# Optimization experiments

Measured on AMD Instinct MI355X. Metric: run time of the kernel, lower is better.

The kernel has to match this reference:

```python
import jax, jax.numpy as jnp
import numpy as np

N = 10000
E = 320000
D = 64


def setup_inputs() -> dict:
    key = jax.random.key(0)
    k1, k2, k3 = jax.random.split(key, 3)
    z = jax.random.normal(k1, (N, D), dtype=jnp.float32)
    edge_index = jax.random.randint(k2, (2, E), 0, N, dtype=jnp.int64)
    W = jax.random.normal(k3, (D, D), dtype=jnp.float32) * (1.0 / np.sqrt(D))
    b = jnp.zeros((D,), dtype=jnp.float32)
    return {"z": z, "edge_index": edge_index, "W": W, "b": b}


def reference(z, edge_index, W, b):
    n = z.shape[0]
    # GCNConv defaults: add self-loops, symmetric normalization D^-1/2 A D^-1/2
    self_loop = jnp.arange(n, dtype=edge_index.dtype)
    row = jnp.concatenate([edge_index[0], self_loop])  # source nodes
    col = jnp.concatenate([edge_index[1], self_loop])  # destination nodes
    deg = jax.ops.segment_sum(jnp.ones_like(col, dtype=z.dtype), col, num_segments=n)
    dinv = jnp.where(deg > 0, jax.lax.rsqrt(deg), 0.0)
    norm = dinv[row] * dinv[col]                        # [E+N]
    h = z @ W                                           # [N, D] linear transform
    msg = h[row] * norm[:, None]                        # gather + scale
    agg = jax.ops.segment_sum(msg, col, num_segments=n) + b  # scatter-add + bias
    zr = jax.nn.relu(agg)
    return zr @ zr.T                                    # [N, N] reconstructed adjacency
```

## Files before the change

### kernel.cpp

```cpp
#include <hip/hip_runtime.h>
#include <math.h>

#define NN 10000
#define NE 320000
#define DD 64
#define TILE 128
#define NTILE 79
#define NPAD (NTILE * TILE)
#define PADROWS (NPAD - NN)
#define NPAIRS (NTILE * (NTILE + 1) / 2)

typedef __bf16 bf16x8 __attribute__((ext_vector_type(8)));
typedef float f32x4 __attribute__((ext_vector_type(4)));

#define OFF_CNT    0
#define OFF_FILL   40064
#define OFF_ROWPTR 80128
#define OFF_SRC    120192
#define OFF_DINV   1400192
#define OFF_H      1440256
#define OFF_ZR1    4000256
#define OFF_ZR2    5294592

__global__ void init_kernel(int* __restrict__ cnt, int* __restrict__ fill,
                            unsigned short* __restrict__ zr1,
                            unsigned short* __restrict__ zr2) {
    int tid = blockIdx.x * 256 + threadIdx.x;
    if (tid < NN) { cnt[tid] = 0; fill[tid] = 0; }
    if (tid < PADROWS * DD) {
        zr1[NN * DD + tid] = 0;
        zr2[NN * DD + tid] = 0;
    }
}

__global__ void count_kernel(const int* __restrict__ ei, int* __restrict__ cnt) {
    int e = blockIdx.x * 256 + threadIdx.x;
    if (e < NE) atomicAdd(&cnt[ei[NE + e]], 1);
}

__global__ void dinv_kernel(const int* __restrict__ cnt, float* __restrict__ dinv) {
    int i = blockIdx.x * 256 + threadIdx.x;
    if (i < NN) dinv[i] = rsqrtf((float)cnt[i] + 1.0f);
}

__global__ __launch_bounds__(256) void scan_kernel(const int* __restrict__ cnt,
                                                   int* __restrict__ rowptr) {
    __shared__ int partial[256];
    const int t = threadIdx.x;
    const int base = t * 40;
    int s = 0;
#pragma unroll 4
    for (int i = 0; i < 40; i++) {
        int idx = base + i;
        if (idx < NN) s += cnt[idx];
    }
    partial[t] = s;
    __syncthreads();
    for (int off = 1; off < 256; off <<= 1) {
        int v = (t >= off) ? partial[t - off] : 0;
        __syncthreads();
        partial[t] += v;
        __syncthreads();
    }
    int run = (t == 0) ? 0 : partial[t - 1];
    for (int i = 0; i < 40; i++) {
        int idx = base + i;
        if (idx < NN) { rowptr[idx] = run; run += cnt[idx]; }
    }
    if (t == 255) rowptr[NN] = partial[255];
}

__global__ void fill_kernel(const int* __restrict__ ei,
                            const int* __restrict__ rowptr,
                            int* __restrict__ fill, int* __restrict__ srcrow) {
    int e = blockIdx.x * 256 + threadIdx.x;
    if (e >= NE) return;
    int c = ei[NE + e];
    int pos = rowptr[c] + atomicAdd(&fill[c], 1);
    srcrow[pos] = ei[e];
}

__global__ __launch_bounds__(256) void h_kernel(const float* __restrict__ z,
                                                const float* __restrict__ W,
                                                float* __restrict__ h) {
    __shared__ float Ws[64 * 64];
    __shared__ float zs[4 * 64];
    const int tid = threadIdx.x;
    const int rbase = blockIdx.x * 4;
#pragma unroll
    for (int i = 0; i < 16; i++) Ws[i * 256 + tid] = W[i * 256 + tid];
    zs[tid] = z[rbase * DD + tid];
    __syncthreads();
    const int r = tid >> 6, d = tid & 63;
    float acc = 0.0f;
#pragma unroll
    for (int k = 0; k < 64; k++) acc = fmaf(zs[r * 64 + k], Ws[k * 64 + d], acc);
    h[(rbase + r) * DD + d] = acc;
}

__global__ __launch_bounds__(256) void agg_kernel(const int* __restrict__ rowptr,
                                                  const int* __restrict__ srcrow,
                                                  const float* __restrict__ dinv,
                                                  const float* __restrict__ h,
                                                  const float* __restrict__ b,
                                                  __bf16* __restrict__ zr1,
                                                  __bf16* __restrict__ zr2) {
    const int lane = threadIdx.x & 63;
    const int n = blockIdx.x * 4 + (threadIdx.x >> 6);
    if (n >= NN) return;
    int s = __builtin_amdgcn_readfirstlane(rowptr[n]);
    int e = __builtin_amdgcn_readfirstlane(rowptr[n + 1]);
    const float dc = dinv[n];
    float acc = 0.0f;
    int i = s;
    for (; i + 1 < e; i += 2) {
        int r0 = __builtin_amdgcn_readfirstlane(srcrow[i]);
        int r1 = __builtin_amdgcn_readfirstlane(srcrow[i + 1]);
        float n0 = dinv[r0] * dc, n1 = dinv[r1] * dc;
        float h0 = h[r0 * DD + lane], h1 = h[r1 * DD + lane];
        acc = fmaf(h0, n0, acc);
        acc = fmaf(h1, n1, acc);
    }
    for (; i < e; i++) {
        int r = __builtin_amdgcn_readfirstlane(srcrow[i]);
        acc = fmaf(h[r * DD + lane], dinv[r] * dc, acc);
    }
    acc = fmaf(h[n * DD + lane], dc * dc, acc) + b[lane];
    acc = acc > 0.0f ? acc : 0.0f;
    __bf16 hi = (__bf16)acc;
    float rem = acc - (float)hi;
    zr1[n * DD + lane] = hi;
    zr2[n * DD + lane] = (__bf16)rem;
}

__global__ __launch_bounds__(256) void gemm_kernel(const __bf16* __restrict__ z1,
                                                   const __bf16* __restrict__ z2,
                                                   float* __restrict__ C) {
    const int t = blockIdx.x;
    const float ff = (float)(2 * NTILE + 1);
    int bi = (int)((ff - sqrtf(ff * ff - 8.0f * (float)t)) * 0.5f);
    while ((bi + 1) * NTILE - ((bi + 1) * bi) / 2 <= t) bi++;
    while (bi * NTILE - (bi * (bi - 1)) / 2 > t) bi--;
    const int bj = bi + (t - (bi * NTILE - (bi * (bi - 1)) / 2));

    const int tid = threadIdx.x;
    const int lane = tid & 63;
    const int w = tid >> 6;
    const int wr = w >> 1, wc = w & 1;
    const int m16 = lane & 15;
    const int kq = lane >> 4;
    const int rbase = bi * TILE + wr * 64;
    const int cbase = bj * TILE + wc * 64;

    f32x4 acc[4][4] = {};

    for (int kk = 0; kk < 2; kk++) {
        const int ko = kk * 32 + kq * 8;
        bf16x8 a1[4], a2[4], b1[4], b2[4];
#pragma unroll
        for (int tt = 0; tt < 4; tt++) {
            const int ar = rbase + tt * 16 + m16;
            const int br = cbase + tt * 16 + m16;
            a1[tt] = *(const bf16x8*)&z1[ar * DD + ko];
            a2[tt] = *(const bf16x8*)&z2[ar * DD + ko];
            b1[tt] = *(const bf16x8*)&z1[br * DD + ko];
            b2[tt] = *(const bf16x8*)&z2[br * DD + ko];
        }
#pragma unroll
        for (int mt = 0; mt < 4; mt++)
#pragma unroll
            for (int nt = 0; nt < 4; nt++) {
                acc[mt][nt] = __builtin_amdgcn_mfma_f32_16x16x32_bf16(a2[mt], b1[nt], acc[mt][nt], 0, 0, 0);
                acc[mt][nt] = __builtin_amdgcn_mfma_f32_16x16x32_bf16(a1[mt], b2[nt], acc[mt][nt], 0, 0, 0);
                acc[mt][nt] = __builtin_amdgcn_mfma_f32_16x16x32_bf16(a1[mt], b1[nt], acc[mt][nt], 0, 0, 0);
            }
    }

#pragma unroll
    for (int mt = 0; mt < 4; mt++) {
        const int row0 = rbase + mt * 16 + kq * 4;
#pragma unroll
        for (int nt = 0; nt < 4; nt++) {
            const int col = cbase + nt * 16 + m16;
            if (col < NN) {
#pragma unroll
                for (int r = 0; r < 4; r++) {
                    const int row = row0 + r;
                    if (row < NN) C[(size_t)row * NN + col] = acc[mt][nt][r];
                }
            }
        }
    }

    if (bi != bj) {
#pragma unroll
        for (int mt = 0; mt < 4; mt++) {
            const int tcol0 = rbase + mt * 16 + kq * 4;
            if (tcol0 < NN) {
#pragma unroll
                for (int nt = 0; nt < 4; nt++) {
                    const int trow = cbase + nt * 16 + m16;
                    if (trow < NN)
                        *(f32x4*)&C[(size_t)trow * NN + tcol0] = acc[mt][nt];
                }
            }
        }
    }
}

extern "C" void kernel_launch(void* const* d_in, const int* in_sizes, int n_in,
                              void* d_out, int out_size, void* d_ws, size_t ws_size,
                              hipStream_t stream) {
    const float* z = (const float*)d_in[0];
    const int* ei = (const int*)d_in[1];
    const float* W = (const float*)d_in[2];
    const float* b = (const float*)d_in[3];
    float* C = (float*)d_out;

    char* ws = (char*)d_ws;
    int* cnt = (int*)(ws + OFF_CNT);
    int* fill = (int*)(ws + OFF_FILL);
    int* rowptr = (int*)(ws + OFF_ROWPTR);
    int* srcrow = (int*)(ws + OFF_SRC);
    float* dinv = (float*)(ws + OFF_DINV);
    float* h = (float*)(ws + OFF_H);
    __bf16* zr1 = (__bf16*)(ws + OFF_ZR1);
    __bf16* zr2 = (__bf16*)(ws + OFF_ZR2);

    init_kernel<<<(NN + 255) / 256, 256, 0, stream>>>(cnt, fill,
                                                      (unsigned short*)zr1,
                                                      (unsigned short*)zr2);
    count_kernel<<<(NE + 255) / 256, 256, 0, stream>>>(ei, cnt);
    dinv_kernel<<<(NN + 255) / 256, 256, 0, stream>>>(cnt, dinv);
    scan_kernel<<<1, 256, 0, stream>>>(cnt, rowptr);
    fill_kernel<<<(NE + 255) / 256, 256, 0, stream>>>(ei, rowptr, fill, srcrow);
    h_kernel<<<NN / 4, 256, 0, stream>>>(z, W, h);
    agg_kernel<<<(NN + 3) / 4, 256, 0, stream>>>(rowptr, srcrow, dinv, h, b, zr1, zr2);

    gemm_kernel<<<NPAIRS, 256, 0, stream>>>(zr1, zr2, C);
}
```

Measured before the change: 544.6 us.

## Fuse preprocessing stages into one cooperative kernel with grid syncs

Replaces seven separate preprocessing launches (init, count, dinv, scan, fill, linear transform, aggregation) with a single cooperative kernel that separates the phases with grid-wide syncs. The scan becomes a two-level block scan across 40 blocks instead of one single-block scan. The aim is to remove per-launch overhead and the serial single-block scan. Grid syncs across 1024 blocks have their own cost, and the bpart scratch aliases the h buffer, which is only safe because h is written after the scan phases. The old launch sequence is kept as a fallback if the cooperative launch fails.

```diff
diff --git a/kernel.cpp b/kernel.cpp
--- a/kernel.cpp
+++ b/kernel.cpp
@@ -1,5 +1,8 @@
 #include <hip/hip_runtime.h>
+#include <hip/hip_cooperative_groups.h>
 #include <math.h>
+
+namespace cg = cooperative_groups;
 
 #define NN 10000
 #define NE 320000
@@ -9,6 +12,7 @@
 #define NPAD (NTILE * TILE)
 #define PADROWS (NPAD - NN)
 #define NPAIRS (NTILE * (NTILE + 1) / 2)
+#define NB 1024
 
 typedef __bf16 bf16x8 __attribute__((ext_vector_type(8)));
 typedef float f32x4 __attribute__((ext_vector_type(4)));
@@ -21,6 +25,125 @@
 #define OFF_H      1440256
 #define OFF_ZR1    4000256
 #define OFF_ZR2    5294592
+
+__global__ __launch_bounds__(256, 4) void preproc_kernel(
+    const float* __restrict__ z, const int* __restrict__ ei,
+    const float* __restrict__ W, const float* __restrict__ bias,
+    int* __restrict__ cnt, int* __restrict__ fill,
+    int* __restrict__ rowptr, int* __restrict__ srcrow,
+    float* __restrict__ dinv, float* __restrict__ h,
+    int* __restrict__ bpart,
+    __bf16* __restrict__ zr1, __bf16* __restrict__ zr2)
+{
+    cg::grid_group grid = cg::this_grid();
+    const int tid = threadIdx.x;
+    const int gtid = blockIdx.x * 256 + tid;
+    const int gstride = NB * 256;
+
+    __shared__ union {
+        struct { float Ws[64 * 64]; float zs[4 * 64]; } hs;
+        int partial[256];
+    } sm;
+
+    for (int i = gtid; i < NN; i += gstride) { cnt[i] = 0; fill[i] = 0; }
+    for (int i = gtid; i < PADROWS * DD; i += gstride) {
+        ((unsigned short*)zr1)[NN * DD + i] = 0;
+        ((unsigned short*)zr2)[NN * DD + i] = 0;
+    }
+    grid.sync();
+
+    for (int e = gtid; e < NE; e += gstride) atomicAdd(&cnt[ei[NE + e]], 1);
+    grid.sync();
+
+    if (blockIdx.x < 40) {
+        const int idx = blockIdx.x * 256 + tid;
+        const int myc = (idx < NN) ? cnt[idx] : 0;
+        if (idx < NN) dinv[idx] = rsqrtf((float)myc + 1.0f);
+        sm.partial[tid] = myc;
+        __syncthreads();
+        for (int off = 1; off < 256; off <<= 1) {
+            int v = (tid >= off) ? sm.partial[tid - off] : 0;
+            __syncthreads();
+            sm.partial[tid] += v;
+            __syncthreads();
+        }
+        if (idx < NN) rowptr[idx] = sm.partial[tid] - myc;
+        if (tid == 255) bpart[blockIdx.x] = sm.partial[255];
+    }
+    grid.sync();
+
+    if (blockIdx.x == 0) {
+        const int v = (tid < 40) ? bpart[tid] : 0;
+        sm.partial[tid] = v;
+        __syncthreads();
+        for (int off = 1; off < 256; off <<= 1) {
+            int vv = (tid >= off) ? sm.partial[tid - off] : 0;
+            __syncthreads();
+            sm.partial[tid] += vv;
+            __syncthreads();
+        }
+        if (tid < 40) bpart[tid] = sm.partial[tid] - v;
+        if (tid == 0) rowptr[NN] = sm.partial[255];
+    }
+    grid.sync();
+
+    if (blockIdx.x < 40) {
+        const int idx = blockIdx.x * 256 + tid;
+        if (idx < NN) rowptr[idx] += bpart[blockIdx.x];
+    }
+    grid.sync();
+
+    for (int e = gtid; e < NE; e += gstride) {
+        int c = ei[NE + e];
+        int pos = rowptr[c] + atomicAdd(&fill[c], 1);
+        srcrow[pos] = ei[e];
+    }
+    grid.sync();
+
+    for (int i = tid; i < 4096; i += 256) sm.hs.Ws[i] = W[i];
+    for (int vb = blockIdx.x; vb < NN / 4; vb += NB) {
+        __syncthreads();
+        sm.hs.zs[tid] = z[vb * 256 + tid];
+        __syncthreads();
+        const int r = tid >> 6, d = tid & 63;
+        float acc = 0.0f;
+#pragma unroll
+        for (int k = 0; k < 64; k++)
+            acc = fmaf(sm.hs.zs[r * 64 + k], sm.hs.Ws[k * 64 + d], acc);
+        h[(vb * 4 + r) * DD + d] = acc;
+    }
+    grid.sync();
+
+    const int lane = tid & 63;
+    for (int g = blockIdx.x; g < (NN + 3) / 4; g += NB) {
+        const int n = g * 4 + (tid >> 6);
+        if (n < NN) {
+            int s = __builtin_amdgcn_readfirstlane(rowptr[n]);
+            int e = __builtin_amdgcn_readfirstlane(rowptr[n + 1]);
+            const float dc = dinv[n];
+            float acc = 0.0f;
+            int i = s;
+            for (; i + 1 < e; i += 2) {
+                int r0 = __builtin_amdgcn_readfirstlane(srcrow[i]);
+                int r1 = __builtin_amdgcn_readfirstlane(srcrow[i + 1]);
+                float n0 = dinv[r0] * dc, n1 = dinv[r1] * dc;
+                float h0 = h[r0 * DD + lane], h1 = h[r1 * DD + lane];
+                acc = fmaf(h0, n0, acc);
+                acc = fmaf(h1, n1, acc);
+            }
+            for (; i < e; i++) {
+                int r = __builtin_amdgcn_readfirstlane(srcrow[i]);
+                acc = fmaf(h[r * DD + lane], dinv[r] * dc, acc);
+            }
+            acc = fmaf(h[n * DD + lane], dc * dc, acc) + bias[lane];
+            acc = acc > 0.0f ? acc : 0.0f;
+            __bf16 hi = (__bf16)acc;
+            float rem = acc - (float)hi;
+            zr1[n * DD + lane] = hi;
+            zr2[n * DD + lane] = (__bf16)rem;
+        }
+    }
+}
 
 __global__ void init_kernel(int* __restrict__ cnt, int* __restrict__ fill,
                             unsigned short* __restrict__ zr1,
@@ -224,18 +347,28 @@
     int* srcrow = (int*)(ws + OFF_SRC);
     float* dinv = (float*)(ws + OFF_DINV);
     float* h = (float*)(ws + OFF_H);
+    int* bpart = (int*)(ws + OFF_H);
     __bf16* zr1 = (__bf16*)(ws + OFF_ZR1);
     __bf16* zr2 = (__bf16*)(ws + OFF_ZR2);
 
-    init_kernel<<<(NN + 255) / 256, 256, 0, stream>>>(cnt, fill,
-                                                      (unsigned short*)zr1,
-                                                      (unsigned short*)zr2);
-    count_kernel<<<(NE + 255) / 256, 256, 0, stream>>>(ei, cnt);
-    dinv_kernel<<<(NN + 255) / 256, 256, 0, stream>>>(cnt, dinv);
-    scan_kernel<<<1, 256, 0, stream>>>(cnt, rowptr);
-    fill_kernel<<<(NE + 255) / 256, 256, 0, stream>>>(ei, rowptr, fill, srcrow);
-    h_kernel<<<NN / 4, 256, 0, stream>>>(z, W, h);
-    agg_kernel<<<(NN + 3) / 4, 256, 0, stream>>>(rowptr, srcrow, dinv, h, b, zr1, zr2);
+    void* args[] = { (void*)&z, (void*)&ei, (void*)&W, (void*)&b,
+                     (void*)&cnt, (void*)&fill, (void*)&rowptr, (void*)&srcrow,
+                     (void*)&dinv, (void*)&h, (void*)&bpart,
+                     (void*)&zr1, (void*)&zr2 };
+    hipError_t err = hipLaunchCooperativeKernel((void*)preproc_kernel,
+                                                dim3(NB), dim3(256),
+                                                args, 0, stream);
+    if (err != hipSuccess) {
+        init_kernel<<<(NN + 255) / 256, 256, 0, stream>>>(cnt, fill,
+                                                          (unsigned short*)zr1,
+                                                          (unsigned short*)zr2);
+        count_kernel<<<(NE + 255) / 256, 256, 0, stream>>>(ei, cnt);
+        dinv_kernel<<<(NN + 255) / 256, 256, 0, stream>>>(cnt, dinv);
+        scan_kernel<<<1, 256, 0, stream>>>(cnt, rowptr);
+        fill_kernel<<<(NE + 255) / 256, 256, 0, stream>>>(ei, rowptr, fill, srcrow);
+        h_kernel<<<NN / 4, 256, 0, stream>>>(z, W, h);
+        agg_kernel<<<(NN + 3) / 4, 256, 0, stream>>>(rowptr, srcrow, dinv, h, b, zr1, zr2);
+    }
 
     gemm_kernel<<<NPAIRS, 256, 0, stream>>>(zr1, zr2, C);
 }
```

After: 1.208 ms. +121.9%, slower.

## Recompute transposed tile and stage output through LDS for coalesced nontemporal stores

Applied to the files above, without the earlier changes.

For off-diagonal tile pairs, the GEMM now recomputes the mirrored tile by swapping operands rather than storing the transpose with strided writes. Each wave stages its accumulator fragments through a shared-memory buffer so that rows can be written to global memory as contiguous 16-byte vectors, using nontemporal stores. The aim is to cut scattered scalar and strided global writes on the output-bound 400 MB store. The cost is doubled MFMA work and input loads for off-diagonal tiles, plus LDS traffic and barriers.

```diff
diff --git a/kernel.cpp b/kernel.cpp
--- a/kernel.cpp
+++ b/kernel.cpp
@@ -136,6 +136,8 @@
 __global__ __launch_bounds__(256) void gemm_kernel(const __bf16* __restrict__ z1,
                                                    const __bf16* __restrict__ z2,
                                                    float* __restrict__ C) {
+    __shared__ float T[4][32][64];
+
     const int t = blockIdx.x;
     const float ff = (float)(2 * NTILE + 1);
     int bi = (int)((ff - sqrtf(ff * ff - 8.0f * (float)t)) * 0.5f);
@@ -149,59 +151,60 @@
     const int wr = w >> 1, wc = w & 1;
     const int m16 = lane & 15;
     const int kq = lane >> 4;
-    const int rbase = bi * TILE + wr * 64;
-    const int cbase = bj * TILE + wc * 64;
-
-    f32x4 acc[4][4] = {};
-
-    for (int kk = 0; kk < 2; kk++) {
-        const int ko = kk * 32 + kq * 8;
-        bf16x8 a1[4], a2[4], b1[4], b2[4];
-#pragma unroll
-        for (int tt = 0; tt < 4; tt++) {
-            const int ar = rbase + tt * 16 + m16;
-            const int br = cbase + tt * 16 + m16;
-            a1[tt] = *(const bf16x8*)&z1[ar * DD + ko];
-            a2[tt] = *(const bf16x8*)&z2[ar * DD + ko];
-            b1[tt] = *(const bf16x8*)&z1[br * DD + ko];
-            b2[tt] = *(const bf16x8*)&z2[br * DD + ko];
+
+    const int norient = (bi == bj) ? 1 : 2;
+    for (int o = 0; o < norient; o++) {
+        const int Ab = (o == 0 ? bi : bj) * TILE + (o == 0 ? wr : wc) * 64;
+        const int Bb = (o == 0 ? bj : bi) * TILE + (o == 0 ? wc : wr) * 64;
+
+        f32x4 acc[4][4] = {};
+        for (int kk = 0; kk < 2; kk++) {
+            const int ko = kk * 32 + kq * 8;
+            bf16x8 a1[4], a2[4], b1[4], b2[4];
+#pragma unroll
+            for (int tt = 0; tt < 4; tt++) {
+                const int ar = Ab + tt * 16 + m16;
+                const int br = Bb + tt * 16 + m16;
+                a1[tt] = *(const bf16x8*)&z1[ar * DD + ko];
+                a2[tt] = *(const bf16x8*)&z2[ar * DD + ko];
+                b1[tt] = *(const bf16x8*)&z1[br * DD + ko];
+                b2[tt] = *(const bf16x8*)&z2[br * DD + ko];
+            }
+#pragma unroll
+            for (int mt = 0; mt < 4; mt++)
+#pragma unroll
+                for (int nt = 0; nt < 4; nt++) {
+                    acc[mt][nt] = __builtin_amdgcn_mfma_f32_16x16x32_bf16(a2[mt], b1[nt], acc[mt][nt], 0, 0, 0);
+                    acc[mt][nt] = __builtin_amdgcn_mfma_f32_16x16x32_bf16(a1[mt], b2[nt], acc[mt][nt], 0, 0, 0);
+                    acc[mt][nt] = __builtin_amdgcn_mfma_f32_16x16x32_bf16(a1[mt], b1[nt], acc[mt][nt], 0, 0, 0);
+                }
         }
-#pragma unroll
-        for (int mt = 0; mt < 4; mt++)
-#pragma unroll
-            for (int nt = 0; nt < 4; nt++) {
-                acc[mt][nt] = __builtin_amdgcn_mfma_f32_16x16x32_bf16(a2[mt], b1[nt], acc[mt][nt], 0, 0, 0);
-                acc[mt][nt] = __builtin_amdgcn_mfma_f32_16x16x32_bf16(a1[mt], b2[nt], acc[mt][nt], 0, 0, 0);
-                acc[mt][nt] = __builtin_amdgcn_mfma_f32_16x16x32_bf16(a1[mt], b1[nt], acc[mt][nt], 0, 0, 0);
-            }
-    }
-
-#pragma unroll
-    for (int mt = 0; mt < 4; mt++) {
-        const int row0 = rbase + mt * 16 + kq * 4;
-#pragma unroll
-        for (int nt = 0; nt < 4; nt++) {
-            const int col = cbase + nt * 16 + m16;
-            if (col < NN) {
-#pragma unroll
-                for (int r = 0; r < 4; r++) {
-                    const int row = row0 + r;
-                    if (row < NN) C[(size_t)row * NN + col] = acc[mt][nt][r];
+
+        for (int hf = 0; hf < 2; hf++) {
+            __syncthreads();
+#pragma unroll
+            for (int mh = 0; mh < 2; mh++) {
+                const int mt = hf * 2 + mh;
+                const int i0 = mh * 16 + kq * 4;
+#pragma unroll
+                for (int nt = 0; nt < 4; nt++) {
+                    const int j = nt * 16 + m16;
+#pragma unroll
+                    for (int r = 0; r < 4; r++)
+                        T[w][i0 + r][j] = acc[mt][nt][r];
                 }
             }
-        }
-    }
-
-    if (bi != bj) {
-#pragma unroll
-        for (int mt = 0; mt < 4; mt++) {
-            const int tcol0 = rbase + mt * 16 + kq * 4;
-            if (tcol0 < NN) {
-#pragma unroll
-                for (int nt = 0; nt < 4; nt++) {
-                    const int trow = cbase + nt * 16 + m16;
-                    if (trow < NN)
-                        *(f32x4*)&C[(size_t)trow * NN + tcol0] = acc[mt][nt];
+            __syncthreads();
+            const int rg = lane >> 4;
+            const int c0 = (lane & 15) * 4;
+#pragma unroll
+            for (int it = 0; it < 8; it++) {
+                const int i = it * 4 + rg;
+                const int grow = Ab + hf * 32 + i;
+                const int gcol = Bb + c0;
+                if (grow < NN && gcol < NN) {
+                    f32x4 v = *(const f32x4*)&T[w][i][c0];
+                    __builtin_nontemporal_store(v, (f32x4*)&C[(size_t)grow * NN + gcol]);
                 }
             }
         }
```

Measured after the change: 538.8 us. Within noise of the previous version (-1.1%).
